# Kernel tuning notes

Measured on AMD Instinct MI355X. Metric: run time of the kernel, lower is better.

The kernel has to match this reference:

```python
import jax, jax.numpy as jnp
import numpy as np

EMBED_DIM = 1024
N_HEADS = 16
HEAD_DIM = EMBED_DIM // N_HEADS
B, N = 4, 2048


def setup_inputs() -> dict:
    key = jax.random.key(0)
    k1, k2, k3, k4, k5 = jax.random.split(key, 5)
    x = jax.random.normal(k1, (B, N, EMBED_DIM), dtype=jnp.float32)
    # Per-head kqv Linear weights stacked: torch Linear(embed_dim, 3*head_dim)
    # torch stores weight as [out, in]; we store transposed [in, out] per head.
    scale = 1.0 / np.sqrt(EMBED_DIM)
    W_kqv = jax.random.uniform(k2, (N_HEADS, EMBED_DIM, 3 * HEAD_DIM), dtype=jnp.float32, minval=-scale, maxval=scale)
    b_kqv = jax.random.uniform(k3, (N_HEADS, 3 * HEAD_DIM), dtype=jnp.float32, minval=-scale, maxval=scale)
    W_proj = jax.random.uniform(k4, (EMBED_DIM, EMBED_DIM), dtype=jnp.float32, minval=-scale, maxval=scale)
    b_proj = jax.random.uniform(k5, (EMBED_DIM,), dtype=jnp.float32, minval=-scale, maxval=scale)
    return {"x": x, "W_kqv": W_kqv, "b_kqv": b_kqv, "W_proj": W_proj, "b_proj": b_proj}


def reference(x, W_kqv, b_kqv, W_proj, b_proj):
    Bx, Nx, D = x.shape
    H = W_kqv.shape[0]
    hd = W_kqv.shape[2] // 3
    # All per-head kqv projections at once: [B, H, N, 3*hd]
    kqv = jnp.einsum('bnd,hde->bhne', x, W_kqv) + b_kqv[None, :, None, :]
    # chunk order in source is (k, q, v)
    k, q, v = jnp.split(kqv, 3, axis=-1)
    # scores scaled by sqrt(head_dim) (D1 in attention_scores is head dim)
    scores = jnp.einsum('bhqd,bhkd->bhqk', q, k) / jnp.sqrt(jnp.float32(hd))
    causal = jnp.tril(jnp.ones((Nx, Nx), dtype=bool))  # [N, N]
    scores = jnp.where(causal[None, None, :, :], scores, -jnp.inf)
    attn = jax.nn.softmax(scores, axis=-1)
    sa = jnp.einsum('bhqk,bhkd->bhqd', attn, v)  # [B, H, N, hd]
    # concat heads along feature dim (head order preserved)
    sa = sa.transpose(0, 2, 1, 3).reshape(Bx, Nx, H * hd)
    # output projection: torch Linear with weight [out, in] -> y = sa @ W^T + b;
    # here W_proj is stored as [in, out]
    return sa @ W_proj + b_proj
```

## Files before the change

kernel.cpp:

```cpp
#include <hip/hip_runtime.h>
#include <math.h>

#define EMBED   1024
#define NHEADS  16
#define HD      64
#define BATCH   4
#define SEQ     2048
#define MROWS   (BATCH*SEQ)
#define NKV     8388608ull

typedef short short8 __attribute__((ext_vector_type(8)));
typedef float floatx4 __attribute__((ext_vector_type(4)));

__device__ __forceinline__ unsigned short f2b(float f) {
    union { float f; unsigned u; } v; v.f = f;
    unsigned r = v.u + 0x7FFFu + ((v.u >> 16) & 1u);
    return (unsigned short)(r >> 16);
}
__device__ __forceinline__ unsigned short f2b_fast(float f) {
    union { float f; unsigned u; } v; v.f = f;
    return (unsigned short)((v.u + 0x8000u) >> 16);
}

#define GLDS16(gp, lp) __builtin_amdgcn_global_load_lds( \
    (const __attribute__((address_space(1))) unsigned int*)(gp), \
    (__attribute__((address_space(3))) unsigned int*)(lp), 16, 0, 0)

__global__ __launch_bounds__(256) void convert_x(
    const float* __restrict__ x, unsigned short* __restrict__ x16)
{
    size_t idx = ((size_t)blockIdx.x * 256 + threadIdx.x) * 8;
    float4 a = *(const float4*)(x + idx);
    float4 b = *(const float4*)(x + idx + 4);
    ushort4 u0, u1;
    u0.x = f2b(a.x); u0.y = f2b(a.y); u0.z = f2b(a.z); u0.w = f2b(a.w);
    u1.x = f2b(b.x); u1.y = f2b(b.y); u1.z = f2b(b.z); u1.w = f2b(b.w);
    *(ushort4*)(x16 + idx) = u0;
    *(ushort4*)(x16 + idx + 4) = u1;
}

__global__ __launch_bounds__(256) void prep_wkqv(
    const float* __restrict__ Wk, unsigned short* __restrict__ Wt)
{
    __shared__ float tile[32][33];
    const int h = blockIdx.z;
    const int k0 = blockIdx.x * 32, e0 = blockIdx.y * 32;
    const float* inh = Wk + (size_t)h * 1024 * 192;
    const int tx = threadIdx.x & 31, ty = threadIdx.x >> 5;
    #pragma unroll
    for (int i = 0; i < 4; i++)
        tile[ty + i * 8][tx] = inh[(size_t)(k0 + ty + i * 8) * 192 + e0 + tx];
    __syncthreads();
    #pragma unroll
    for (int i = 0; i < 4; i++) {
        int e = e0 + ty + i * 8;
        int cp = (e >> 6) * 1024 + h * 64 + (e & 63);
        Wt[(size_t)cp * 1024 + k0 + tx] = f2b(tile[tx][ty + i * 8]);
    }
}

__global__ __launch_bounds__(256) void transpose_w(
    const float* __restrict__ in, unsigned short* __restrict__ outp, int R, int C)
{
    __shared__ float tile[32][33];
    const int r0 = blockIdx.x * 32, c0 = blockIdx.y * 32;
    const int tx = threadIdx.x & 31, ty = threadIdx.x >> 5;
    #pragma unroll
    for (int i = 0; i < 4; i++)
        tile[ty + i * 8][tx] = in[(size_t)(r0 + ty + i * 8) * C + c0 + tx];
    __syncthreads();
    #pragma unroll
    for (int i = 0; i < 4; i++)
        outp[(size_t)(c0 + ty + i * 8) * R + r0 + tx] = f2b(tile[tx][ty + i * 8]);
}

__device__ __forceinline__ void mainloop_128x256(
    const unsigned short* __restrict__ Ag,
    const unsigned short* __restrict__ Bg,
    unsigned short* smem,
    int row0, int col0, floatx4 (&acc)[4][4])
{
    const int t = threadIdx.x;
    const int wave = t >> 6, lane = t & 63;
    const int lr = lane & 15, quad = lane >> 4;
    const int wr = wave >> 2, wc = wave & 3;
    const int swz8 = ((lane & 7) ^ ((lane >> 3) & 7)) * 8;
    const int c0 = (quad ^ (lr & 7)) * 8;
    const int c1 = ((4 + quad) ^ (lr & 7)) * 8;

    #pragma unroll
    for (int m = 0; m < 4; m++)
        #pragma unroll
        for (int n = 0; n < 4; n++) acc[m][n] = (floatx4){0.f, 0.f, 0.f, 0.f};

#define STG(G, R0, KC, L) do { \
    _Pragma("unroll") \
    for (int i_ = 0; i_ < 2; i_++) { \
        int rl_ = i_ * 64 + wave * 8 + (lane >> 3); \
        GLDS16((G) + (size_t)((R0) + rl_) * 1024 + (KC) + swz8, \
               (L) + rl_ * 64 + (lane & 7) * 8); \
    } } while (0)

    unsigned short* const a0 = smem;
    unsigned short* const a1 = smem + 8192;
    unsigned short* const a2 = smem + 16384;
    unsigned short* const b0 = smem + 24576;
    unsigned short* const b1 = smem + 24576 + 16384;
    unsigned short* const b2 = smem + 24576 + 32768;

#define KTILE(J, AR, BR, AT, BT) do { \
    const unsigned short* pA_ = (AR) + (wr * 64 + lr) * 64; \
    const unsigned short* pB_ = (BR) + (wc * 64 + lr) * 64; \
    short8 af0[4], af1[4], b0f[4], b1f[4]; \
    _Pragma("unroll") \
    for (int m = 0; m < 4; m++) { \
        af0[m] = *(const short8*)(pA_ + m * 1024 + c0); \
        af1[m] = *(const short8*)(pA_ + m * 1024 + c1); \
    } \
    _Pragma("unroll") \
    for (int n = 0; n < 4; n++) { \
        b0f[n] = *(const short8*)(pB_ + n * 1024 + c0); \
        b1f[n] = *(const short8*)(pB_ + n * 1024 + c1); \
    } \
    if ((J) < 14) { \
        STG(Ag, row0,       ((J) + 2) * 64, (AT)); \
        STG(Bg, col0,       ((J) + 2) * 64, (BT)); \
        STG(Bg, col0 + 128, ((J) + 2) * 64, (BT) + 8192); \
    } \
    asm volatile("s_waitcnt lgkmcnt(0)" ::: "memory"); \
    __builtin_amdgcn_s_setprio(1); \
    _Pragma("unroll") \
    for (int m = 0; m < 4; m++) \
        _Pragma("unroll") \
        for (int n = 0; n < 4; n++) \
            acc[m][n] = __builtin_amdgcn_mfma_f32_16x16x32_bf16(af0[m], b0f[n], acc[m][n], 0, 0, 0); \
    _Pragma("unroll") \
    for (int m = 0; m < 4; m++) \
        _Pragma("unroll") \
        for (int n = 0; n < 4; n++) \
            acc[m][n] = __builtin_amdgcn_mfma_f32_16x16x32_bf16(af1[m], b1f[n], acc[m][n], 0, 0, 0); \
    __builtin_amdgcn_s_setprio(0); \
    if ((J) < 14)       { asm volatile("s_waitcnt vmcnt(6)" ::: "memory"); } \
    else if ((J) == 14) { asm volatile("s_waitcnt vmcnt(0)" ::: "memory"); } \
    __builtin_amdgcn_s_barrier(); \
} while (0)

    STG(Ag, row0,       0,  a0);
    STG(Bg, col0,       0,  b0);
    STG(Bg, col0 + 128, 0,  b0 + 8192);
    STG(Ag, row0,       64, a1);
    STG(Bg, col0,       64, b1);
    STG(Bg, col0 + 128, 64, b1 + 8192);
    asm volatile("s_waitcnt vmcnt(6)" ::: "memory");
    __builtin_amdgcn_s_barrier();

    for (int j0 = 0; j0 < 15; j0 += 3) {
        KTILE(j0,     a0, b0, a2, b2);
        KTILE(j0 + 1, a1, b1, a0, b0);
        KTILE(j0 + 2, a2, b2, a1, b1);
    }
    KTILE(15, a0, b0, a2, b2);
#undef KTILE
#undef STG
}

__global__ __launch_bounds__(512, 2) void gemm_kqv(
    const unsigned short* __restrict__ A,
    const unsigned short* __restrict__ Bt,
    const float* __restrict__ bk,
    unsigned short* __restrict__ Kb16,
    unsigned short* __restrict__ Qb16,
    unsigned short* __restrict__ Vt16)
{
    __shared__ unsigned short smem[73728];

    const int mt = blockIdx.x;
    const int ct = blockIdx.y;
    const int row0 = mt * 128, col0 = ct * 256;

    floatx4 acc[4][4];
    mainloop_128x256(A, Bt, smem, row0, col0, acc);

    const int t = threadIdx.x;
    const int wave = t >> 6, lane = t & 63;
    const int lr = lane & 15, quad = lane >> 4;
    const int wr = wave >> 2, wc = wave & 3;

    unsigned short* W = smem + wave * 4096;
    const int sec = ct >> 2;
    const int h = ((ct & 3) << 2) + wc;
    const int bidx = row0 >> 11;
    const int rbase = (row0 & 2047) + wr * 64;

    float bias[4];
    #pragma unroll
    for (int n = 0; n < 4; n++) bias[n] = bk[h * 192 + sec * 64 + n * 16 + lr];

    if (sec < 2) {
        const float scl = (sec == 1) ? (0.125f * 1.44269504089f) : 1.0f;
        #pragma unroll
        for (int m = 0; m < 4; m++)
            #pragma unroll
            for (int n = 0; n < 4; n++) {
                int es = (n * 16 + lr) ^ (quad << 4);
                #pragma unroll
                for (int r = 0; r < 4; r++)
                    W[(m * 16 + quad * 4 + r) * 64 + es] = f2b((acc[m][n][r] + bias[n]) * scl);
            }
        __syncthreads();
        unsigned short* dst = ((sec == 0) ? Kb16 : Qb16)
                              + ((size_t)(bidx * 16 + h) * 2048 + rbase) * 64;
        const int rrow = lane >> 3, chunk = lane & 7;
        #pragma unroll
        for (int p = 0; p < 8; p++) {
            int row = p * 8 + rrow;
            int ch = chunk ^ (((row >> 2) & 3) << 1);
            *(float4*)(dst + (size_t)row * 64 + chunk * 8) =
                *(const float4*)(W + row * 64 + ch * 8);
        }
    } else {
        #pragma unroll
        for (int m = 0; m < 4; m++)
            #pragma unroll
            for (int n = 0; n < 4; n++) {
                int e = n * 16 + lr;
                ushort4 pk;
                pk.x = f2b(acc[m][n][0] + bias[n]);
                pk.y = f2b(acc[m][n][1] + bias[n]);
                pk.z = f2b(acc[m][n][2] + bias[n]);
                pk.w = f2b(acc[m][n][3] + bias[n]);
                int mp = m ^ (lr & 3);
                *(ushort4*)(W + e * 64 + mp * 16 + quad * 4) = pk;
            }
        __syncthreads();
        unsigned short* dstV = Vt16 + (size_t)(bidx * 16 + h) * 64 * 2048 + rbase;
        const int ev = lane >> 3, chunkR = lane & 7;
        #pragma unroll
        for (int p = 0; p < 8; p++) {
            int e = p * 8 + ev;
            int ch = chunkR ^ ((e & 3) << 1);
            *(float4*)(dstV + (size_t)e * 2048 + chunkR * 8) =
                *(const float4*)(W + e * 64 + ch * 8);
        }
    }
}

__global__ __launch_bounds__(256, 2) void attn_mfma(
    const unsigned short* __restrict__ Kb,
    const unsigned short* __restrict__ Qb,
    const unsigned short* __restrict__ Vt,
    unsigned short* __restrict__ sa)
{
    const int bh = blockIdx.x;
    const int bx = blockIdx.y;
    const int b = bh >> 4, h = bh & 15;
    const int wave = threadIdx.x >> 6;
    const int lane = threadIdx.x & 63;
    const int lr = lane & 15, quad = lane >> 4;
    const int qt_[2] = {bx, 15 - bx};

    __shared__ unsigned short Ks[2][64 * 64];
    __shared__ unsigned short Vs[2][64 * 64];
    __shared__ unsigned short Ps[4][2][16 * 72];

    const unsigned short* Kbh = Kb + (size_t)bh * 2048 * 64;
    const unsigned short* Vbh = Vt + (size_t)bh * 64 * 2048;
    const unsigned short* Qbh = Qb + (size_t)bh * 2048 * 64;

    short8 qf[2][2][2];
    #pragma unroll
    for (int tt = 0; tt < 2; tt++)
        #pragma unroll
        for (int s = 0; s < 2; s++) {
            const unsigned short* qp = Qbh +
                (size_t)(qt_[tt] * 128 + wave * 32 + s * 16 + lr) * 64 + quad * 8;
            qf[tt][s][0] = *(const short8*)(qp);
            qf[tt][s][1] = *(const short8*)(qp + 32);
        }

    floatx4 O[2][2][4];
    float ls[2][2][4];
    #pragma unroll
    for (int tt = 0; tt < 2; tt++)
        #pragma unroll
        for (int s = 0; s < 2; s++) {
            #pragma unroll
            for (int d = 0; d < 4; d++) O[tt][s][d] = (floatx4){0.f, 0.f, 0.f, 0.f};
            #pragma unroll
            for (int r = 0; r < 4; r++) ls[tt][s][r] = 0.f;
        }

    const int r_local = lane >> 3, cc = lane & 7;
    const int swz = cc ^ r_local;
    const int whalf = wave >> 1;

#define STAGE_KV(KT, BSEL) do { \
    const int k0_ = (KT) * 64; \
    _Pragma("unroll") \
    for (int j_ = 0; j_ < 2; j_++) { \
        int R_ = wave * 16 + j_ * 8 + r_local; \
        GLDS16(Kbh + (size_t)(k0_ + R_) * 64 + swz * 8, \
               &Ks[BSEL][0] + (wave * 16 + j_ * 8) * 64 + lane * 8); \
        GLDS16(Vbh + (size_t)R_ * 2048 + k0_ + swz * 8, \
               &Vs[BSEL][0] + (wave * 16 + j_ * 8) * 64 + lane * 8); \
    } } while (0)

    const int ktmax = 2 * qt_[1] + 1;

    STAGE_KV(0, 0);
    asm volatile("s_waitcnt vmcnt(0)" ::: "memory");
    __builtin_amdgcn_s_barrier();

    for (int kt = 0; kt <= ktmax; kt++) {
        const int buf = kt & 1;
        const unsigned short* Ksb = &Ks[buf][0];
        const unsigned short* Vsb = &Vs[buf][0];
        const int k0 = kt * 64;

        if (kt < ktmax) {
            if (buf) STAGE_KV(kt + 1, 0);
            else     STAGE_KV(kt + 1, 1);
        }

        #pragma unroll
        for (int tt = 0; tt < 2; tt++) {
            const int qt2 = qt_[tt];
            const int lim = 2 * qt2 + whalf;
            if (kt > lim) continue;

            floatx4 S[2][4];
            #pragma unroll
            for (int s = 0; s < 2; s++)
                #pragma unroll
                for (int a = 0; a < 4; a++) S[s][a] = (floatx4){0.f, 0.f, 0.f, 0.f};
            #pragma unroll
            for (int c = 0; c < 2; c++)
                #pragma unroll
                for (int a = 0; a < 4; a++) {
                    int R = a * 16 + lr;
                    short8 kf = *(const short8*)(Ksb + R * 64 + (((c * 4 + quad) ^ (lr & 7)) * 8));
                    #pragma unroll
                    for (int s = 0; s < 2; s++)
                        S[s][a] = __builtin_amdgcn_mfma_f32_16x16x32_bf16(qf[tt][s][c], kf, S[s][a], 0, 0, 0);
                }

            if (kt == lim) {
                #pragma unroll
                for (int s = 0; s < 2; s++)
                    #pragma unroll
                    for (int a = 0; a < 4; a++) {
                        int col = k0 + a * 16 + lr;
                        #pragma unroll
                        for (int r = 0; r < 4; r++) {
                            int grow = qt2 * 128 + wave * 32 + s * 16 + quad * 4 + r;
                            if (col > grow) S[s][a][r] = -INFINITY;
                        }
                    }
            }

            #pragma unroll
            for (int s = 0; s < 2; s++)
                #pragma unroll
                for (int a = 0; a < 4; a++)
                    #pragma unroll
                    for (int r = 0; r < 4; r++) {
                        float p = __builtin_amdgcn_exp2f(S[s][a][r]);
                        ls[tt][s][r] += p;
                        Ps[wave][s][(quad * 4 + r) * 72 + a * 16 + lr] = f2b_fast(p);
                    }

            short8 pa[2][2];
            #pragma unroll
            for (int s = 0; s < 2; s++)
                #pragma unroll
                for (int c = 0; c < 2; c++)
                    pa[s][c] = *(const short8*)(Ps[wave][s] + lr * 72 + c * 32 + quad * 8);

            #pragma unroll
            for (int c = 0; c < 2; c++)
                #pragma unroll
                for (int d = 0; d < 4; d++) {
                    int R = d * 16 + lr;
                    short8 vf = *(const short8*)(Vsb + R * 64 + (((c * 4 + quad) ^ (lr & 7)) * 8));
                    #pragma unroll
                    for (int s = 0; s < 2; s++)
                        O[tt][s][d] = __builtin_amdgcn_mfma_f32_16x16x32_bf16(pa[s][c], vf, O[tt][s][d], 0, 0, 0);
                }
        }

        asm volatile("s_waitcnt vmcnt(0)" ::: "memory");
        __builtin_amdgcn_s_barrier();
    }
#undef STAGE_KV

    #pragma unroll
    for (int tt = 0; tt < 2; tt++)
        #pragma unroll
        for (int s = 0; s < 2; s++)
            #pragma unroll
            for (int r = 0; r < 4; r++) {
                float sm = ls[tt][s][r];
                sm += __shfl_xor(sm, 1);
                sm += __shfl_xor(sm, 2);
                sm += __shfl_xor(sm, 4);
                sm += __shfl_xor(sm, 8);
                float inv = 1.0f / sm;
                size_t base = ((size_t)(b * 2048 + qt_[tt] * 128 + wave * 32 + s * 16 + quad * 4 + r)) * 1024
                              + h * 64 + lr;
                #pragma unroll
                for (int d = 0; d < 4; d++)
                    sa[base + d * 16] = f2b(O[tt][s][d][r] * inv);
            }
}

__global__ __launch_bounds__(512, 2) void gemm_proj(
    const unsigned short* __restrict__ A,
    const unsigned short* __restrict__ Bt,
    const float* __restrict__ bp,
    float* __restrict__ out)
{
    __shared__ unsigned short smem[73728];

    const int mt = blockIdx.x;
    const int ct = blockIdx.y;
    const int row0 = mt * 128, col0 = ct * 256;

    floatx4 acc[4][4];
    mainloop_128x256(A, Bt, smem, row0, col0, acc);

    const int t = threadIdx.x;
    const int lane = t & 63, wave = t >> 6;
    const int lr = lane & 15, quad = lane >> 4;
    const int wr = wave >> 2, wc = wave & 3;

    float bias[4]; int cols[4];
    #pragma unroll
    for (int n = 0; n < 4; n++) {
        cols[n] = col0 + wc * 64 + n * 16 + lr;
        bias[n] = bp[cols[n]];
    }
    #pragma unroll
    for (int a = 0; a < 4; a++) {
        #pragma unroll
        for (int n = 0; n < 4; n++) {
            #pragma unroll
            for (int r = 0; r < 4; r++) {
                int m = row0 + wr * 64 + a * 16 + quad * 4 + r;
                out[(size_t)m * 1024 + cols[n]] = acc[a][n][r] + bias[n];
            }
        }
    }
}

extern "C" void kernel_launch(void* const* d_in, const int* in_sizes, int n_in,
                              void* d_out, int out_size, void* d_ws, size_t ws_size,
                              hipStream_t stream) {
    const float* x  = (const float*)d_in[0];
    const float* Wk = (const float*)d_in[1];
    const float* bk = (const float*)d_in[2];
    const float* Wp = (const float*)d_in[3];
    const float* bp = (const float*)d_in[4];
    float* out = (float*)d_out;

    unsigned short* Kb16 = (unsigned short*)d_ws;
    unsigned short* Qb16 = Kb16 + NKV;
    unsigned short* Vt16 = Qb16 + NKV;
    unsigned short* sa16 = Vt16 + NKV;
    unsigned short* x16  = sa16 + 8388608ull;
    unsigned short* Wt   = x16  + 8388608ull;
    unsigned short* Wpt  = Wt   + 3145728ull;

    convert_x<<<4096, 256, 0, stream>>>(x, x16);
    prep_wkqv<<<dim3(32, 6, 16), 256, 0, stream>>>(Wk, Wt);
    transpose_w<<<dim3(32, 32, 1), 256, 0, stream>>>(Wp, Wpt, 1024, 1024);
    gemm_kqv<<<dim3(64, 12), 512, 0, stream>>>(x16, Wt, bk, Kb16, Qb16, Vt16);
    attn_mfma<<<dim3(64, 8), 256, 0, stream>>>(Kb16, Qb16, Vt16, sa16);
    gemm_proj<<<dim3(64, 4), 512, 0, stream>>>(sa16, Wpt, bp, out);
}
```

Measured before the change: 235.7 us.

## Merge prep kernels into one launch; split attention into one q-tile per block

The three preprocessing kernels (x conversion, Wkqv transpose, Wproj transpose) are combined into a single launch that dispatches on block index, removing two kernel launches. The attention kernel no longer pairs a light and a heavy causal q-tile per block. Each block now handles one 128-row q-tile, the grid doubles to 1024 blocks with heavy tiles scheduled first, and launch bounds allow 3 blocks per CU. This trades balanced per-block work for more parallelism and lower register pressure, at the cost of each block reloading its own K/V.

Measured after the change: 222.4 us (median of 2 runs). -5.6%, faster.

```diff
diff --git a/kernel.cpp b/kernel.cpp
--- a/kernel.cpp
+++ b/kernel.cpp
@@ -26,52 +26,56 @@
     (const __attribute__((address_space(1))) unsigned int*)(gp), \
     (__attribute__((address_space(3))) unsigned int*)(lp), 16, 0, 0)
 
-__global__ __launch_bounds__(256) void convert_x(
-    const float* __restrict__ x, unsigned short* __restrict__ x16)
-{
-    size_t idx = ((size_t)blockIdx.x * 256 + threadIdx.x) * 8;
-    float4 a = *(const float4*)(x + idx);
-    float4 b = *(const float4*)(x + idx + 4);
-    ushort4 u0, u1;
-    u0.x = f2b(a.x); u0.y = f2b(a.y); u0.z = f2b(a.z); u0.w = f2b(a.w);
-    u1.x = f2b(b.x); u1.y = f2b(b.y); u1.z = f2b(b.z); u1.w = f2b(b.w);
-    *(ushort4*)(x16 + idx) = u0;
-    *(ushort4*)(x16 + idx + 4) = u1;
-}
-
-__global__ __launch_bounds__(256) void prep_wkqv(
-    const float* __restrict__ Wk, unsigned short* __restrict__ Wt)
+__global__ __launch_bounds__(256) void prepass(
+    const float* __restrict__ x,  unsigned short* __restrict__ x16,
+    const float* __restrict__ Wk, unsigned short* __restrict__ Wt,
+    const float* __restrict__ Wp, unsigned short* __restrict__ Wpt)
 {
     __shared__ float tile[32][33];
-    const int h = blockIdx.z;
-    const int k0 = blockIdx.x * 32, e0 = blockIdx.y * 32;
-    const float* inh = Wk + (size_t)h * 1024 * 192;
+    const int bid = blockIdx.x;
+
+    if (bid < 4096) {
+        size_t idx = ((size_t)bid * 256 + threadIdx.x) * 8;
+        float4 a = *(const float4*)(x + idx);
+        float4 b = *(const float4*)(x + idx + 4);
+        ushort4 u0, u1;
+        u0.x = f2b(a.x); u0.y = f2b(a.y); u0.z = f2b(a.z); u0.w = f2b(a.w);
+        u1.x = f2b(b.x); u1.y = f2b(b.y); u1.z = f2b(b.z); u1.w = f2b(b.w);
+        *(ushort4*)(x16 + idx) = u0;
+        *(ushort4*)(x16 + idx + 4) = u1;
+        return;
+    }
+
     const int tx = threadIdx.x & 31, ty = threadIdx.x >> 5;
-    #pragma unroll
-    for (int i = 0; i < 4; i++)
-        tile[ty + i * 8][tx] = inh[(size_t)(k0 + ty + i * 8) * 192 + e0 + tx];
-    __syncthreads();
-    #pragma unroll
-    for (int i = 0; i < 4; i++) {
-        int e = e0 + ty + i * 8;
-        int cp = (e >> 6) * 1024 + h * 64 + (e & 63);
-        Wt[(size_t)cp * 1024 + k0 + tx] = f2b(tile[tx][ty + i * 8]);
-    }
-}
-
-__global__ __launch_bounds__(256) void transpose_w(
-    const float* __restrict__ in, unsigned short* __restrict__ outp, int R, int C)
-{
-    __shared__ float tile[32][33];
-    const int r0 = blockIdx.x * 32, c0 = blockIdx.y * 32;
-    const int tx = threadIdx.x & 31, ty = threadIdx.x >> 5;
-    #pragma unroll
-    for (int i = 0; i < 4; i++)
-        tile[ty + i * 8][tx] = in[(size_t)(r0 + ty + i * 8) * C + c0 + tx];
-    __syncthreads();
-    #pragma unroll
-    for (int i = 0; i < 4; i++)
-        outp[(size_t)(c0 + ty + i * 8) * R + r0 + tx] = f2b(tile[tx][ty + i * 8]);
+    if (bid < 7168) {
+        const int bb = bid - 4096;
+        const int h = bb / 192;
+        const int k0 = (bb & 31) * 32, e0 = ((bb >> 5) % 6) * 32;
+        const float* inh = Wk + (size_t)h * 1024 * 192;
+        #pragma unroll
+        for (int i = 0; i < 4; i++)
+            tile[ty + i * 8][tx] = inh[(size_t)(k0 + ty + i * 8) * 192 + e0 + tx];
+        __syncthreads();
+        #pragma unroll
+        for (int i = 0; i < 4; i++) {
+            int e = e0 + ty + i * 8;
+            int cp = (e >> 6) * 1024 + h * 64 + (e & 63);
+            Wt[(size_t)cp * 1024 + k0 + tx] = f2b(tile[tx][ty + i * 8]);
+        }
+        return;
+    }
+
+    {
+        const int bb = bid - 7168;
+        const int r0 = (bb & 31) * 32, c0 = (bb >> 5) * 32;
+        #pragma unroll
+        for (int i = 0; i < 4; i++)
+            tile[ty + i * 8][tx] = Wp[(size_t)(r0 + ty + i * 8) * 1024 + c0 + tx];
+        __syncthreads();
+        #pragma unroll
+        for (int i = 0; i < 4; i++)
+            Wpt[(size_t)(c0 + ty + i * 8) * 1024 + r0 + tx] = f2b(tile[tx][ty + i * 8]);
+    }
 }
 
 __device__ __forceinline__ void mainloop_128x256(
@@ -245,19 +249,18 @@
     }
 }
 
-__global__ __launch_bounds__(256, 2) void attn_mfma(
+__global__ __launch_bounds__(256, 3) void attn_mfma(
     const unsigned short* __restrict__ Kb,
     const unsigned short* __restrict__ Qb,
     const unsigned short* __restrict__ Vt,
     unsigned short* __restrict__ sa)
 {
     const int bh = blockIdx.x;
-    const int bx = blockIdx.y;
+    const int qt = 15 - blockIdx.y;
     const int b = bh >> 4, h = bh & 15;
     const int wave = threadIdx.x >> 6;
     const int lane = threadIdx.x & 63;
     const int lr = lane & 15, quad = lane >> 4;
-    const int qt_[2] = {bx, 15 - bx};
 
     __shared__ unsigned short Ks[2][64 * 64];
     __shared__ unsigned short Vs[2][64 * 64];
@@ -267,28 +270,24 @@
     const unsigned short* Vbh = Vt + (size_t)bh * 64 * 2048;
     const unsigned short* Qbh = Qb + (size_t)bh * 2048 * 64;
 
-    short8 qf[2][2][2];
-    #pragma unroll
-    for (int tt = 0; tt < 2; tt++)
-        #pragma unroll
-        for (int s = 0; s < 2; s++) {
-            const unsigned short* qp = Qbh +
-                (size_t)(qt_[tt] * 128 + wave * 32 + s * 16 + lr) * 64 + quad * 8;
-            qf[tt][s][0] = *(const short8*)(qp);
-            qf[tt][s][1] = *(const short8*)(qp + 32);
-        }
-
-    floatx4 O[2][2][4];
-    float ls[2][2][4];
-    #pragma unroll
-    for (int tt = 0; tt < 2; tt++)
-        #pragma unroll
-        for (int s = 0; s < 2; s++) {
-            #pragma unroll
-            for (int d = 0; d < 4; d++) O[tt][s][d] = (floatx4){0.f, 0.f, 0.f, 0.f};
-            #pragma unroll
-            for (int r = 0; r < 4; r++) ls[tt][s][r] = 0.f;
-        }
+    short8 qf[2][2];
+    #pragma unroll
+    for (int s = 0; s < 2; s++) {
+        const unsigned short* qp = Qbh +
+            (size_t)(qt * 128 + wave * 32 + s * 16 + lr) * 64 + quad * 8;
+        qf[s][0] = *(const short8*)(qp);
+        qf[s][1] = *(const short8*)(qp + 32);
+    }
+
+    floatx4 O[2][4];
+    float ls[2][4];
+    #pragma unroll
+    for (int s = 0; s < 2; s++) {
+        #pragma unroll
+        for (int d = 0; d < 4; d++) O[s][d] = (floatx4){0.f, 0.f, 0.f, 0.f};
+        #pragma unroll
+        for (int r = 0; r < 4; r++) ls[s][r] = 0.f;
+    }
 
     const int r_local = lane >> 3, cc = lane & 7;
     const int swz = cc ^ r_local;
@@ -305,7 +304,8 @@
                &Vs[BSEL][0] + (wave * 16 + j_ * 8) * 64 + lane * 8); \
     } } while (0)
 
-    const int ktmax = 2 * qt_[1] + 1;
+    const int ktmax = 2 * qt + 1;
+    const int lim = 2 * qt + whalf;
 
     STAGE_KV(0, 0);
     asm volatile("s_waitcnt vmcnt(0)" ::: "memory");
@@ -322,12 +322,7 @@
             else     STAGE_KV(kt + 1, 1);
         }
 
-        #pragma unroll
-        for (int tt = 0; tt < 2; tt++) {
-            const int qt2 = qt_[tt];
-            const int lim = 2 * qt2 + whalf;
-            if (kt > lim) continue;
-
+        if (kt <= lim) {
             floatx4 S[2][4];
             #pragma unroll
             for (int s = 0; s < 2; s++)
@@ -341,7 +336,7 @@
                     short8 kf = *(const short8*)(Ksb + R * 64 + (((c * 4 + quad) ^ (lr & 7)) * 8));
                     #pragma unroll
                     for (int s = 0; s < 2; s++)
-                        S[s][a] = __builtin_amdgcn_mfma_f32_16x16x32_bf16(qf[tt][s][c], kf, S[s][a], 0, 0, 0);
+                        S[s][a] = __builtin_amdgcn_mfma_f32_16x16x32_bf16(qf[s][c], kf, S[s][a], 0, 0, 0);
                 }
 
             if (kt == lim) {
@@ -352,7 +347,7 @@
                         int col = k0 + a * 16 + lr;
                         #pragma unroll
                         for (int r = 0; r < 4; r++) {
-                            int grow = qt2 * 128 + wave * 32 + s * 16 + quad * 4 + r;
+                            int grow = qt * 128 + wave * 32 + s * 16 + quad * 4 + r;
                             if (col > grow) S[s][a][r] = -INFINITY;
                         }
                     }
@@ -365,7 +360,7 @@
                     #pragma unroll
                     for (int r = 0; r < 4; r++) {
                         float p = __builtin_amdgcn_exp2f(S[s][a][r]);
-                        ls[tt][s][r] += p;
+                        ls[s][r] += p;
                         Ps[wave][s][(quad * 4 + r) * 72 + a * 16 + lr] = f2b_fast(p);
                     }
 
@@ -384,7 +379,7 @@
                     short8 vf = *(const short8*)(Vsb + R * 64 + (((c * 4 + quad) ^ (lr & 7)) * 8));
                     #pragma unroll
                     for (int s = 0; s < 2; s++)
-                        O[tt][s][d] = __builtin_amdgcn_mfma_f32_16x16x32_bf16(pa[s][c], vf, O[tt][s][d], 0, 0, 0);
+                        O[s][d] = __builtin_amdgcn_mfma_f32_16x16x32_bf16(pa[s][c], vf, O[s][d], 0, 0, 0);
                 }
         }
 
@@ -394,23 +389,21 @@
 #undef STAGE_KV
 
     #pragma unroll
-    for (int tt = 0; tt < 2; tt++)
-        #pragma unroll
-        for (int s = 0; s < 2; s++)
-            #pragma unroll
-            for (int r = 0; r < 4; r++) {
-                float sm = ls[tt][s][r];
-                sm += __shfl_xor(sm, 1);
-                sm += __shfl_xor(sm, 2);
-                sm += __shfl_xor(sm, 4);
-                sm += __shfl_xor(sm, 8);
-                float inv = 1.0f / sm;
-                size_t base = ((size_t)(b * 2048 + qt_[tt] * 128 + wave * 32 + s * 16 + quad * 4 + r)) * 1024
-                              + h * 64 + lr;
-                #pragma unroll
-                for (int d = 0; d < 4; d++)
-                    sa[base + d * 16] = f2b(O[tt][s][d][r] * inv);
-            }
+    for (int s = 0; s < 2; s++)
+        #pragma unroll
+        for (int r = 0; r < 4; r++) {
+            float sm = ls[s][r];
+            sm += __shfl_xor(sm, 1);
+            sm += __shfl_xor(sm, 2);
+            sm += __shfl_xor(sm, 4);
+            sm += __shfl_xor(sm, 8);
+            float inv = 1.0f / sm;
+            size_t base = ((size_t)(b * 2048 + qt * 128 + wave * 32 + s * 16 + quad * 4 + r)) * 1024
+                          + h * 64 + lr;
+            #pragma unroll
+            for (int d = 0; d < 4; d++)
+                sa[base + d * 16] = f2b(O[s][d][r] * inv);
+        }
 }
 
 __global__ __launch_bounds__(512, 2) void gemm_proj(
@@ -470,10 +463,8 @@
     unsigned short* Wt   = x16  + 8388608ull;
     unsigned short* Wpt  = Wt   + 3145728ull;
 
-    convert_x<<<4096, 256, 0, stream>>>(x, x16);
-    prep_wkqv<<<dim3(32, 6, 16), 256, 0, stream>>>(Wk, Wt);
-    transpose_w<<<dim3(32, 32, 1), 256, 0, stream>>>(Wp, Wpt, 1024, 1024);
+    prepass<<<8192, 256, 0, stream>>>(x, x16, Wk, Wt, Wp, Wpt);
     gemm_kqv<<<dim3(64, 12), 512, 0, stream>>>(x16, Wt, bk, Kb16, Qb16, Vt16);
-    attn_mfma<<<dim3(64, 8), 256, 0, stream>>>(Kb16, Qb16, Vt16, sa16);
+    attn_mfma<<<dim3(64, 16), 256, 0, stream>>>(Kb16, Qb16, Vt16, sa16);
     gemm_proj<<<dim3(64, 4), 512, 0, stream>>>(sa16, Wpt, bp, out);
 }
```
